# Kernel optimization log

Measured on AMD Instinct MI355X. Metric: run time of the kernel, lower is better.

## Reference

```python
import jax, jax.numpy as jnp
import numpy as np
import math

D_MODEL, N_HEADS, D_FF = 512, 8, 2048
B, S = 4, 2048
EPS = 1e-6


def _layernorm(x, alpha, bias):
    # Faithful to the torch module: std is unbiased (ddof=1) and eps is added to std, not var.
    m = jnp.mean(x, axis=-1, keepdims=True)
    s = jnp.std(x, axis=-1, keepdims=True, ddof=1)
    return alpha * (x - m) / (s + EPS) + bias


def setup_inputs() -> dict:
    key = jax.random.key(0)
    ks = jax.random.split(key, 16)
    d, f = D_MODEL, D_FF
    sd = 1.0 / math.sqrt(d)
    sf = 1.0 / math.sqrt(f)
    return {
        "x": jax.random.normal(ks[0], (B, S, d), jnp.float32),
        "wq": jax.random.normal(ks[1], (d, d), jnp.float32) * sd,
        "bq": jnp.zeros((d,), jnp.float32),
        "wk": jax.random.normal(ks[2], (d, d), jnp.float32) * sd,
        "bk": jnp.zeros((d,), jnp.float32),
        "wv": jax.random.normal(ks[3], (d, d), jnp.float32) * sd,
        "bv": jnp.zeros((d,), jnp.float32),
        "wo": jax.random.normal(ks[4], (d, d), jnp.float32) * sd,
        "bo": jnp.zeros((d,), jnp.float32),
        "w1": jax.random.normal(ks[5], (d, f), jnp.float32) * sd,
        "b1": jnp.zeros((f,), jnp.float32),
        "w2": jax.random.normal(ks[6], (f, d), jnp.float32) * sf,
        "b2": jnp.zeros((d,), jnp.float32),
        "ln1_a": jnp.ones((d,), jnp.float32),
        "ln1_b": jnp.zeros((d,), jnp.float32),
        "ln2_a": jnp.ones((d,), jnp.float32),
        "ln2_b": jnp.zeros((d,), jnp.float32),
    }


def reference(x, wq, bq, wk, bk, wv, bv, wo, bo, w1, b1, w2, b2, ln1_a, ln1_b, ln2_a, ln2_b):
    b, s, d = x.shape
    h, dk = N_HEADS, d // N_HEADS
    # QKV projections -> [b, h, s, dk]
    q = (x @ wq + bq).reshape(b, s, h, dk).transpose(0, 2, 1, 3)
    k = (x @ wk + bk).reshape(b, s, h, dk).transpose(0, 2, 1, 3)
    v = (x @ wv + bv).reshape(b, s, h, dk).transpose(0, 2, 1, 3)
    # Manual scaled-dot-product attention (no mask in EncoderBlock path)
    scores = jnp.einsum("bhqd,bhkd->bhqk", q, k) / jnp.sqrt(jnp.float32(dk))
    probs = jax.nn.softmax(scores, axis=-1)
    attn = jnp.einsum("bhqk,bhkd->bhqd", probs, v)
    concat = attn.transpose(0, 2, 1, 3).reshape(b, s, d)
    mha_out = concat @ wo + bo
    # Residual + LayerNorm 1
    y = _layernorm(x + mha_out, ln1_a, ln1_b)
    # FFN + Residual + LayerNorm 2
    ff = jax.nn.relu(y @ w1 + b1) @ w2 + b2
    return _layernorm(y + ff, ln2_a, ln2_b)
```

## Files before the change

kernel.cpp:

```cpp
#include <hip/hip_runtime.h>
#include <hip/hip_bf16.h>


typedef __bf16 bf16;
typedef __bf16 bf16x4 __attribute__((ext_vector_type(4)));
typedef __bf16 bf16x8 __attribute__((ext_vector_type(8)));
typedef float  f32x4  __attribute__((ext_vector_type(4)));

#define NBATCH 4
#define SEQ    2048
#define DMODEL 512
#define NHEADS 8
#define DHEAD  64
#define DFF    2048
#define MTOT   (NBATCH * SEQ)
#define WS_NEED 73416712u

__device__ __forceinline__ f32x4 mfma16(bf16x8 a, bf16x8 b, f32x4 c) {
    return __builtin_amdgcn_mfma_f32_16x16x32_bf16(a, b, c, 0, 0, 0);
}

__device__ __forceinline__ void lds16(const bf16* g, bf16* l) {
    __builtin_amdgcn_global_load_lds(
        (const __attribute__((address_space(1))) void*)g,
        (__attribute__((address_space(3))) void*)l, 16, 0, 0);
}

__device__ __forceinline__ float scrub(float f) {
    return (fabsf(f) < 1e30f) ? f : 0.f;
}

__global__ void sentinel_kernel(bf16* out) {
    out[threadIdx.x] = (bf16)1000.0f;
}

__global__ __launch_bounds__(256) void convert_x(
        const float* __restrict__ src, bf16* __restrict__ dst) {
    int i = (blockIdx.x * 256 + threadIdx.x) * 4;
    float4 f = *(const float4*)(src + i);
    bf16x4 o = {(bf16)scrub(f.x), (bf16)scrub(f.y),
                (bf16)scrub(f.z), (bf16)scrub(f.w)};
    *(bf16x4*)(dst + i) = o;
}

__global__ __launch_bounds__(256) void prep_kernel(
        const float* wq, const float* wk, const float* wv, const float* wo,
        const float* w1, const float* w2,
        const float* bq, const float* bk, const float* bv, const float* bo,
        const float* b1, const float* b2,
        const float* l1a, const float* l1b, const float* l2a, const float* l2b,
        bf16* __restrict__ wT, bf16* __restrict__ w1T, bf16* __restrict__ w2T,
        bf16* __restrict__ prm) {
    __shared__ bf16 tile[32][33];
    int b = blockIdx.x;
    if (b < 10) {
        const float* srcs[10] = {bq, bk, bv, bo, b1, b2, l1a, l1b, l2a, l2b};
        const int len[10] = {512,512,512,512,2048,512,512,512,512,512};
        const int dst[10] = {0,512,1024,1536,2048,4096,4608,5120,5632,6144};
        const float* s = srcs[b];
        bf16* d = prm + dst[b];
        for (int i = threadIdx.x; i < len[b]; i += 256)
            d[i] = (bf16)scrub(s[i]);
        return;
    }
    const float* in; bf16* out; int K, N, bx, by;
    if (b < 1034) {
        int idx = b - 10, z = idx >> 8, rem = idx & 255;
        const float* srcs[4] = {wq, wk, wv, wo};
        in = srcs[z]; out = wT + (size_t)z * 262144;
        K = 512; N = 512; bx = rem & 15; by = rem >> 4;
    } else if (b < 2058) {
        int idx = b - 1034;
        in = w1; out = w1T; K = 512; N = 2048; bx = idx & 63; by = idx >> 6;
    } else {
        int idx = b - 2058;
        in = w2; out = w2T; K = 2048; N = 512; bx = idx & 15; by = idx >> 4;
    }
    int tx = threadIdx.x & 31, ty = threadIdx.x >> 5;
    int n0 = bx * 32, k0 = by * 32;
#pragma unroll
    for (int i = 0; i < 4; i++) {
        int kl = ty * 4 + i;
        tile[kl][tx] = (bf16)scrub(in[(size_t)(k0 + kl) * N + n0 + tx]);
    }
    __syncthreads();
#pragma unroll
    for (int i = 0; i < 4; i++) {
        int nl = ty * 4 + i;
        out[(size_t)(n0 + nl) * K + k0 + tx] = tile[tx][nl];
    }
}

template <bool RELU>
__global__ __launch_bounds__(256) void gemm_bt(
        const bf16* __restrict__ A, const bf16* __restrict__ BT,
        const bf16* __restrict__ bias, bf16* __restrict__ Cout,
        int M, int N, int K) {
    constexpr int BM = 128, BN = 128, BK = 32;
    __shared__ __align__(16) bf16 As[BM * BK];
    __shared__ __align__(16) bf16 Bs[BN * BK];

    int tid  = threadIdx.x;
    int wid  = tid >> 6, lane = tid & 63;
    int quad = lane >> 4, l15 = lane & 15;
    int mb = blockIdx.x * BM, nb = blockIdx.y * BN;
    int wm = (wid >> 1) * 64, wn = (wid & 1) * 64;

    f32x4 acc[4][4] = {};

    int c0 = wid * 128 + lane, c1 = c0 + 64;
    int ar0 = c0 >> 2, ac0 = (c0 & 3) * 8;
    int ar1 = c1 >> 2, ac1 = (c1 & 3) * 8;
    bf16* lA0 = &As[(wid * 2 + 0) * 512];
    bf16* lA1 = &As[(wid * 2 + 1) * 512];
    bf16* lB0 = &Bs[(wid * 2 + 0) * 512];
    bf16* lB1 = &Bs[(wid * 2 + 1) * 512];

    for (int k0 = 0; k0 < K; k0 += BK) {
        __syncthreads();
        lds16(&A [(size_t)(mb + ar0) * K + k0 + ac0], lA0);
        lds16(&A [(size_t)(mb + ar1) * K + k0 + ac1], lA1);
        lds16(&BT[(size_t)(nb + ar0) * K + k0 + ac0], lB0);
        lds16(&BT[(size_t)(nb + ar1) * K + k0 + ac1], lB1);
        __syncthreads();

        bf16x8 af[4], bfr[4];
#pragma unroll
        for (int i = 0; i < 4; i++)
            af[i] = *(const bf16x8*)&As[(wm + i * 16 + l15) * 32 + quad * 8];
#pragma unroll
        for (int j = 0; j < 4; j++)
            bfr[j] = *(const bf16x8*)&Bs[(wn + j * 16 + l15) * 32 + quad * 8];
#pragma unroll
        for (int i = 0; i < 4; i++)
#pragma unroll
            for (int j = 0; j < 4; j++)
                acc[i][j] = mfma16(af[i], bfr[j], acc[i][j]);
    }

#pragma unroll
    for (int j = 0; j < 4; j++) {
        int n = nb + wn + j * 16 + l15;
        float bv = (float)bias[n];
#pragma unroll
        for (int i = 0; i < 4; i++) {
            int mBase = mb + wm + i * 16 + quad * 4;
#pragma unroll
            for (int r = 0; r < 4; r++) {
                float v = acc[i][j][r] + bv;
                if (RELU) v = v > 0.f ? v : 0.f;
                Cout[(size_t)(mBase + r) * N + n] = (bf16)v;
            }
        }
    }
}

template <bool RELU>
__global__ __launch_bounds__(256) void gemm_bt64(
        const bf16* __restrict__ A, const bf16* __restrict__ BT,
        const bf16* __restrict__ bias, bf16* __restrict__ Cout,
        int M, int N, int K) {
    constexpr int BM = 64, BN = 128, BK = 32;
    __shared__ __align__(16) bf16 As[BM * BK];
    __shared__ __align__(16) bf16 Bs[BN * BK];

    int tid  = threadIdx.x;
    int wid  = tid >> 6, lane = tid & 63;
    int quad = lane >> 4, l15 = lane & 15;
    int mb = blockIdx.x * BM, nb = blockIdx.y * BN;
    int wm = (wid >> 1) * 32, wn = (wid & 1) * 64;

    f32x4 acc[2][4] = {};

    int cA = wid * 64 + lane;
    int arA = cA >> 2, acA = (cA & 3) * 8;
    int cB0 = wid * 128 + lane, cB1 = cB0 + 64;
    int br0 = cB0 >> 2, bc0 = (cB0 & 3) * 8;
    int br1 = cB1 >> 2, bc1 = (cB1 & 3) * 8;
    bf16* lA  = &As[wid * 512];
    bf16* lB0 = &Bs[(wid * 2 + 0) * 512];
    bf16* lB1 = &Bs[(wid * 2 + 1) * 512];

    for (int k0 = 0; k0 < K; k0 += BK) {
        __syncthreads();
        lds16(&A [(size_t)(mb + arA) * K + k0 + acA], lA);
        lds16(&BT[(size_t)(nb + br0) * K + k0 + bc0], lB0);
        lds16(&BT[(size_t)(nb + br1) * K + k0 + bc1], lB1);
        __syncthreads();

        bf16x8 af[2], bfr[4];
#pragma unroll
        for (int i = 0; i < 2; i++)
            af[i] = *(const bf16x8*)&As[(wm + i * 16 + l15) * 32 + quad * 8];
#pragma unroll
        for (int j = 0; j < 4; j++)
            bfr[j] = *(const bf16x8*)&Bs[(wn + j * 16 + l15) * 32 + quad * 8];
#pragma unroll
        for (int i = 0; i < 2; i++)
#pragma unroll
            for (int j = 0; j < 4; j++)
                acc[i][j] = mfma16(af[i], bfr[j], acc[i][j]);
    }

#pragma unroll
    for (int j = 0; j < 4; j++) {
        int n = nb + wn + j * 16 + l15;
        float bv = (float)bias[n];
#pragma unroll
        for (int i = 0; i < 2; i++) {
            int mBase = mb + wm + i * 16 + quad * 4;
#pragma unroll
            for (int r = 0; r < 4; r++) {
                float v = acc[i][j][r] + bv;
                if (RELU) v = v > 0.f ? v : 0.f;
                Cout[(size_t)(mBase + r) * N + n] = (bf16)v;
            }
        }
    }
}

__global__ __launch_bounds__(256) void gemm_qkv(
        const bf16* __restrict__ A, const bf16* __restrict__ BT,
        const bf16* __restrict__ bias,
        bf16* __restrict__ Cq, bf16* __restrict__ Ck, bf16* __restrict__ Cv,
        int M, int N, int K) {
    constexpr int BM = 128, BN = 128, BK = 32;
    __shared__ __align__(16) bf16 As[BM * BK];
    __shared__ __align__(16) bf16 Bs[BN * BK];
    __shared__ __align__(16) bf16 Ts[128 * 136];

    int tid  = threadIdx.x;
    int wid  = tid >> 6, lane = tid & 63;
    int quad = lane >> 4, l15 = lane & 15;
    int mb = blockIdx.x * BM, nb = blockIdx.y * BN;
    int wm = (wid >> 1) * 64, wn = (wid & 1) * 64;

    f32x4 acc[4][4] = {};

    int c0 = wid * 128 + lane, c1 = c0 + 64;
    int ar0 = c0 >> 2, ac0 = (c0 & 3) * 8;
    int ar1 = c1 >> 2, ac1 = (c1 & 3) * 8;
    bf16* lA0 = &As[(wid * 2 + 0) * 512];
    bf16* lA1 = &As[(wid * 2 + 1) * 512];
    bf16* lB0 = &Bs[(wid * 2 + 0) * 512];
    bf16* lB1 = &Bs[(wid * 2 + 1) * 512];

    for (int k0 = 0; k0 < K; k0 += BK) {
        __syncthreads();
        lds16(&A [(size_t)(mb + ar0) * K + k0 + ac0], lA0);
        lds16(&A [(size_t)(mb + ar1) * K + k0 + ac1], lA1);
        lds16(&BT[(size_t)(nb + ar0) * K + k0 + ac0], lB0);
        lds16(&BT[(size_t)(nb + ar1) * K + k0 + ac1], lB1);
        __syncthreads();

        bf16x8 af[4], bfr[4];
#pragma unroll
        for (int i = 0; i < 4; i++)
            af[i] = *(const bf16x8*)&As[(wm + i * 16 + l15) * 32 + quad * 8];
#pragma unroll
        for (int j = 0; j < 4; j++)
            bfr[j] = *(const bf16x8*)&Bs[(wn + j * 16 + l15) * 32 + quad * 8];
#pragma unroll
        for (int i = 0; i < 4; i++)
#pragma unroll
            for (int j = 0; j < 4; j++)
                acc[i][j] = mfma16(af[i], bfr[j], acc[i][j]);
    }

    int reg = nb >> 9;
    if (reg < 2) {
        bf16* C = reg ? Ck : Cq;
        float scl = reg ? 1.0f : 0.125f;
#pragma unroll
        for (int j = 0; j < 4; j++) {
            int n = nb + wn + j * 16 + l15;
            float bv = (float)bias[n];
            int nn = n & 511;
            int h = nn >> 6, dk = nn & 63;
#pragma unroll
            for (int i = 0; i < 4; i++) {
                int mBase = mb + wm + i * 16 + quad * 4;
#pragma unroll
                for (int r = 0; r < 4; r++) {
                    float v = (acc[i][j][r] + bv) * scl;
                    int m = mBase + r;
                    int b = m >> 11, s = m & (SEQ - 1);
                    C[((size_t)(b * NHEADS + h) * SEQ + s) * DHEAD + dk] = (bf16)v;
                }
            }
        }
    } else {
#pragma unroll
        for (int j = 0; j < 4; j++) {
            int nl = wn + j * 16 + l15;
            float bv = (float)bias[nb + nl];
#pragma unroll
            for (int i = 0; i < 4; i++) {
                int ml = wm + i * 16 + quad * 4;
                bf16x4 pk;
#pragma unroll
                for (int r = 0; r < 4; r++) pk[r] = (bf16)(acc[i][j][r] + bv);
                *(bf16x4*)&Ts[nl * 136 + ml] = pk;
            }
        }
        __syncthreads();
        int nl = tid >> 1, half = tid & 1;
        int nn = (nb + nl) & 511;
        int h = nn >> 6, dk = nn & 63;
        int bb = mb >> 11, s0 = mb & (SEQ - 1);
        bf16* dst = &Cv[((size_t)(bb * NHEADS + h) * DHEAD + dk) * SEQ + s0 + half * 64];
        const bf16* srcl = &Ts[nl * 136 + half * 64];
#pragma unroll
        for (int v = 0; v < 8; v++)
            *(uint4*)(dst + v * 8) = *(const uint4*)(srcl + v * 8);
    }
}

__global__ __launch_bounds__(256) void attn_kernel(
        const bf16* __restrict__ Q, const bf16* __restrict__ K,
        const bf16* __restrict__ VT, bf16* __restrict__ Out) {
    __shared__ __align__(16) bf16 Ks[2][64 * 72];
    __shared__ __align__(16) bf16 Vs[2][64 * 72];
    __shared__ __align__(16) bf16 Pb[4][2][16 * 72];
    int tid  = threadIdx.x;
    int wid  = tid >> 6, lane = tid & 63;
    int quad = lane >> 4, l15 = lane & 15;
    int bh = blockIdx.y;
    int qb = blockIdx.x * 128 + wid * 32;

    const bf16* Qh = Q  + (size_t)bh * SEQ * DHEAD;
    const bf16* Kh = K  + (size_t)bh * SEQ * DHEAD;
    const bf16* Vh = VT + (size_t)bh * DHEAD * SEQ;

    bf16x8 bQ0[2], bQ1[2];
#pragma unroll
    for (int c = 0; c < 2; c++) {
        const bf16* qp = &Qh[(qb + c * 16 + l15) * DHEAD + quad * 8];
        bQ0[c] = *(const bf16x8*)qp;
        bQ1[c] = *(const bf16x8*)(qp + 32);
    }

    int cc0 = tid * 2, cc1 = cc0 + 1;
    int kr0 = cc0 >> 3, kc0 = (cc0 & 7) * 8;
    int kr1 = cc1 >> 3, kc1 = (cc1 & 7) * 8;

    float lrow[2] = {0.f, 0.f};
    f32x4 Oacc[2][4] = {};

    {
        uint4 ka0 = *(const uint4*)&Kh[(size_t)kr0 * DHEAD + kc0];
        uint4 ka1 = *(const uint4*)&Kh[(size_t)kr1 * DHEAD + kc1];
        uint4 va0 = *(const uint4*)&Vh[(size_t)kr0 * SEQ + kc0];
        uint4 va1 = *(const uint4*)&Vh[(size_t)kr1 * SEQ + kc1];
        *(uint4*)&Ks[0][kr0 * 72 + kc0] = ka0;
        *(uint4*)&Ks[0][kr1 * 72 + kc1] = ka1;
        *(uint4*)&Vs[0][kr0 * 72 + kc0] = va0;
        *(uint4*)&Vs[0][kr1 * 72 + kc1] = va1;
    }
    __syncthreads();

    for (int it = 0; it < SEQ / 64; it++) {
        int cur = it & 1, nxt = cur ^ 1;
        int kb = (it + 1) * 64;
        uint4 nk0, nk1, nv0, nv1;
        bool pf = (it + 1 < SEQ / 64);
        if (pf) {
            nk0 = *(const uint4*)&Kh[(size_t)(kb + kr0) * DHEAD + kc0];
            nk1 = *(const uint4*)&Kh[(size_t)(kb + kr1) * DHEAD + kc1];
            nv0 = *(const uint4*)&Vh[(size_t)kr0 * SEQ + kb + kc0];
            nv1 = *(const uint4*)&Vh[(size_t)kr1 * SEQ + kb + kc1];
        }

        bf16x8 aK0[4], aK1[4], bV0[4], bV1[4];
#pragma unroll
        for (int t = 0; t < 4; t++) {
            const bf16* kp = &Ks[cur][(t * 16 + l15) * 72 + quad * 8];
            aK0[t] = *(const bf16x8*)kp;
            aK1[t] = *(const bf16x8*)(kp + 32);
            const bf16* vp = &Vs[cur][(t * 16 + l15) * 72 + quad * 8];
            bV0[t] = *(const bf16x8*)vp;
            bV1[t] = *(const bf16x8*)(vp + 32);
        }

#pragma unroll
        for (int c = 0; c < 2; c++) {
            f32x4 st[4];
#pragma unroll
            for (int t = 0; t < 4; t++) {
                f32x4 z = {0.f, 0.f, 0.f, 0.f};
                st[t] = mfma16(aK1[t], bQ1[c], mfma16(aK0[t], bQ0[c], z));
            }
            bf16* myP = Pb[wid][c];
#pragma unroll
            for (int t = 0; t < 4; t++) {
                bf16x4 pk;
                float ps = 0.f;
#pragma unroll
                for (int r = 0; r < 4; r++) {
                    float p = __expf(fminf(st[t][r], 60.f));
                    ps += p;
                    pk[r] = (bf16)p;
                }
                lrow[c] += ps;
                *(bf16x4*)&myP[l15 * 72 + t * 16 + quad * 4] = pk;
            }
            bf16x8 aP0 = *(const bf16x8*)&myP[l15 * 72 + quad * 8];
            bf16x8 aP1 = *(const bf16x8*)&myP[l15 * 72 + 32 + quad * 8];
#pragma unroll
            for (int nt = 0; nt < 4; nt++)
                Oacc[c][nt] = mfma16(aP1, bV1[nt],
                                     mfma16(aP0, bV0[nt], Oacc[c][nt]));
        }

        if (pf) {
            *(uint4*)&Ks[nxt][kr0 * 72 + kc0] = nk0;
            *(uint4*)&Ks[nxt][kr1 * 72 + kc1] = nk1;
            *(uint4*)&Vs[nxt][kr0 * 72 + kc0] = nv0;
            *(uint4*)&Vs[nxt][kr1 * 72 + kc1] = nv1;
        }
        __syncthreads();
    }

    int b = bh >> 3, hd = bh & 7;
#pragma unroll
    for (int c = 0; c < 2; c++) {
        float l = lrow[c];
        l += __shfl_xor(l, 16);
        l += __shfl_xor(l, 32);
        float linv[4];
#pragma unroll
        for (int r = 0; r < 4; r++)
            linv[r] = 1.f / __shfl(l, quad * 4 + r);
#pragma unroll
        for (int nt = 0; nt < 4; nt++)
#pragma unroll
            for (int r = 0; r < 4; r++) {
                int s = qb + c * 16 + quad * 4 + r;
                Out[((size_t)(b * SEQ + s)) * DMODEL + hd * 64 + nt * 16 + l15]
                    = (bf16)(Oacc[c][nt][r] * linv[r]);
            }
    }
}

__global__ __launch_bounds__(256) void ln_kernel(
        const bf16* __restrict__ X, const bf16* __restrict__ T,
        const bf16* __restrict__ Al, const bf16* __restrict__ Bl,
        void* __restrict__ Out, int final_out) {
    int wid = threadIdx.x >> 6, lane = threadIdx.x & 63;
    int row = blockIdx.x * 4 + wid;
    const bf16* xr = X + (size_t)row * DMODEL;
    const bf16* tr = T + (size_t)row * DMODEL;
    bf16x8 xv = *(const bf16x8*)&xr[lane * 8];
    bf16x8 tv = *(const bf16x8*)&tr[lane * 8];
    float v[8];
#pragma unroll
    for (int i = 0; i < 8; i++) v[i] = (float)xv[i] + (float)tv[i];
    float sum = 0.f, sq = 0.f;
#pragma unroll
    for (int i = 0; i < 8; i++) { sum += v[i]; sq += v[i] * v[i]; }
#pragma unroll
    for (int m = 1; m < 64; m <<= 1) {
        sum += __shfl_xor(sum, m);
        sq  += __shfl_xor(sq,  m);
    }
    float mean = sum * (1.f / DMODEL);
    float var  = (sq - DMODEL * mean * mean) * (1.f / (DMODEL - 1));
    var = var > 0.f ? var : 0.f;
    float inv = 1.f / (sqrtf(var) + 1e-6f);
#pragma unroll
    for (int i = 0; i < 8; i++) {
        int c = lane * 8 + i;
        float yv = (float)Al[c] * (v[i] - mean) * inv + (float)Bl[c];
        yv = fminf(fmaxf(yv, -1e4f), 1e4f);
        size_t idx = (size_t)row * DMODEL + c;
        if (final_out) ((float*)Out)[idx] = yv;
        else           ((bf16*)Out)[idx]  = (bf16)yv;
    }
}

extern "C" void kernel_launch(void* const* d_in, const int* in_sizes, int n_in,
                              void* d_out, int out_size, void* d_ws, size_t ws_size,
                              hipStream_t stream) {
    if (ws_size < WS_NEED) {
        sentinel_kernel<<<1, 64, 0, stream>>>((bf16*)d_out);
        return;
    }

    const float* x  = (const float*)d_in[0];
    const float* wq = (const float*)d_in[1],  *bq = (const float*)d_in[2];
    const float* wk = (const float*)d_in[3],  *bk = (const float*)d_in[4];
    const float* wv = (const float*)d_in[5],  *bv = (const float*)d_in[6];
    const float* wo = (const float*)d_in[7],  *bo = (const float*)d_in[8];
    const float* w1 = (const float*)d_in[9],  *b1 = (const float*)d_in[10];
    const float* w2 = (const float*)d_in[11], *b2 = (const float*)d_in[12];
    const float* ln1a = (const float*)d_in[13], *ln1b = (const float*)d_in[14];
    const float* ln2a = (const float*)d_in[15], *ln2b = (const float*)d_in[16];

    char* ws = (char*)d_ws;
    bf16* wT   = (bf16*)(ws + 0);
    bf16* woT  = (bf16*)(ws + 1572864);
    bf16* w1T  = (bf16*)(ws + 2097152);
    bf16* w2T  = (bf16*)(ws + 4194304);
    bf16* xcv  = (bf16*)(ws + 6291456);
    bf16* prm  = (bf16*)(ws + 14680064);
    bf16* regA = (bf16*)(ws + 14696448);
    bf16* regB = (bf16*)(ws + 23085056);
    bf16* regC = (bf16*)(ws + 31473664);
    bf16* ff1  = (bf16*)(ws + 39862272);
    bf16* aout = (bf16*)d_out;

    bf16 *pbq = prm, *pbo = prm + 1536;
    bf16 *pb1 = prm + 2048, *pb2 = prm + 4096;
    bf16 *pl1a = prm + 4608, *pl1b = prm + 5120;
    bf16 *pl2a = prm + 5632, *pl2b = prm + 6144;

    convert_x<<<4096, 256, 0, stream>>>(x, xcv);
    prep_kernel<<<3082, 256, 0, stream>>>(wq, wk, wv, wo, w1, w2,
                                          bq, bk, bv, bo, b1, b2,
                                          ln1a, ln1b, ln2a, ln2b,
                                          wT, w1T, w2T, prm);

    gemm_qkv<<<dim3(64, 12), 256, 0, stream>>>(xcv, wT, pbq,
                                               regA, regB, regC,
                                               MTOT, 3 * DMODEL, DMODEL);

    attn_kernel<<<dim3(SEQ / 128, NBATCH * NHEADS), 256, 0, stream>>>(
        regA, regB, regC, aout);

    gemm_bt64<false><<<dim3(128, 4), 256, 0, stream>>>(aout, woT, pbo, regA,
                                                       MTOT, DMODEL, DMODEL);

    ln_kernel<<<MTOT / 4, 256, 0, stream>>>(xcv, regA, pl1a, pl1b, regB, 0);

    gemm_bt<true ><<<dim3(64, 16), 256, 0, stream>>>(regB, w1T, pb1, ff1,
                                                     MTOT, DFF, DMODEL);
    gemm_bt64<false><<<dim3(128, 4), 256, 0, stream>>>(ff1, w2T, pb2, regA,
                                                       MTOT, DMODEL, DFF);

    ln_kernel<<<MTOT / 4, 256, 0, stream>>>(regB, regA, pl2a, pl2b, d_out, 1);
}
```

Measured before the change: 293.0 us.

## Split attention across key halves with merge kernel, fuse x conversion, widen GEMM K-step

Attention now runs two blocks per query tile, each covering half the keys. They write unnormalised fp32 partial outputs and row sums, which a new merge kernel combines and normalises into bf16. The intent is to raise parallelism and occupancy in the attention stage, at the cost of extra fp32 partial traffic and one more launch. The x conversion is folded into the weight-prep kernel to save a launch. The bt64 GEMM loads 64-wide K slices per barrier pair to halve synchronisation.

```diff
diff --git a/kernel.cpp b/kernel.cpp
--- a/kernel.cpp
+++ b/kernel.cpp
@@ -14,7 +14,7 @@
 #define DHEAD  64
 #define DFF    2048
 #define MTOT   (NBATCH * SEQ)
-#define WS_NEED 73416712u
+#define WS_NEED 73940992u
 
 __device__ __forceinline__ f32x4 mfma16(bf16x8 a, bf16x8 b, f32x4 c) {
     return __builtin_amdgcn_mfma_f32_16x16x32_bf16(a, b, c, 0, 0, 0);
@@ -34,46 +34,48 @@
     out[threadIdx.x] = (bf16)1000.0f;
 }
 
-__global__ __launch_bounds__(256) void convert_x(
-        const float* __restrict__ src, bf16* __restrict__ dst) {
-    int i = (blockIdx.x * 256 + threadIdx.x) * 4;
-    float4 f = *(const float4*)(src + i);
-    bf16x4 o = {(bf16)scrub(f.x), (bf16)scrub(f.y),
-                (bf16)scrub(f.z), (bf16)scrub(f.w)};
-    *(bf16x4*)(dst + i) = o;
-}
-
 __global__ __launch_bounds__(256) void prep_kernel(
+        const float* x,
         const float* wq, const float* wk, const float* wv, const float* wo,
         const float* w1, const float* w2,
         const float* bq, const float* bk, const float* bv, const float* bo,
         const float* b1, const float* b2,
         const float* l1a, const float* l1b, const float* l2a, const float* l2b,
+        bf16* __restrict__ xcv,
         bf16* __restrict__ wT, bf16* __restrict__ w1T, bf16* __restrict__ w2T,
         bf16* __restrict__ prm) {
     __shared__ bf16 tile[32][33];
     int b = blockIdx.x;
-    if (b < 10) {
+    if (b < 4096) {
+        int i = (b * 256 + threadIdx.x) * 4;
+        float4 f = *(const float4*)(x + i);
+        bf16x4 o = {(bf16)scrub(f.x), (bf16)scrub(f.y),
+                    (bf16)scrub(f.z), (bf16)scrub(f.w)};
+        *(bf16x4*)(xcv + i) = o;
+        return;
+    }
+    if (b < 4106) {
+        int pb = b - 4096;
         const float* srcs[10] = {bq, bk, bv, bo, b1, b2, l1a, l1b, l2a, l2b};
         const int len[10] = {512,512,512,512,2048,512,512,512,512,512};
         const int dst[10] = {0,512,1024,1536,2048,4096,4608,5120,5632,6144};
-        const float* s = srcs[b];
-        bf16* d = prm + dst[b];
-        for (int i = threadIdx.x; i < len[b]; i += 256)
+        const float* s = srcs[pb];
+        bf16* d = prm + dst[pb];
+        for (int i = threadIdx.x; i < len[pb]; i += 256)
             d[i] = (bf16)scrub(s[i]);
         return;
     }
     const float* in; bf16* out; int K, N, bx, by;
-    if (b < 1034) {
-        int idx = b - 10, z = idx >> 8, rem = idx & 255;
+    if (b < 5130) {
+        int idx = b - 4106, z = idx >> 8, rem = idx & 255;
         const float* srcs[4] = {wq, wk, wv, wo};
         in = srcs[z]; out = wT + (size_t)z * 262144;
         K = 512; N = 512; bx = rem & 15; by = rem >> 4;
-    } else if (b < 2058) {
-        int idx = b - 1034;
+    } else if (b < 6154) {
+        int idx = b - 5130;
         in = w1; out = w1T; K = 512; N = 2048; bx = idx & 63; by = idx >> 6;
     } else {
-        int idx = b - 2058;
+        int idx = b - 6154;
         in = w2; out = w2T; K = 2048; N = 512; bx = idx & 15; by = idx >> 4;
     }
     int tx = threadIdx.x & 31, ty = threadIdx.x >> 5;
@@ -160,9 +162,9 @@
         const bf16* __restrict__ A, const bf16* __restrict__ BT,
         const bf16* __restrict__ bias, bf16* __restrict__ Cout,
         int M, int N, int K) {
-    constexpr int BM = 64, BN = 128, BK = 32;
-    __shared__ __align__(16) bf16 As[BM * BK];
-    __shared__ __align__(16) bf16 Bs[BN * BK];
+    constexpr int BM = 64, BN = 128;
+    __shared__ __align__(16) bf16 As0[BM * 32], As1[BM * 32];
+    __shared__ __align__(16) bf16 Bs0[BN * 32], Bs1[BN * 32];
 
     int tid  = threadIdx.x;
     int wid  = tid >> 6, lane = tid & 63;
@@ -177,29 +179,39 @@
     int cB0 = wid * 128 + lane, cB1 = cB0 + 64;
     int br0 = cB0 >> 2, bc0 = (cB0 & 3) * 8;
     int br1 = cB1 >> 2, bc1 = (cB1 & 3) * 8;
-    bf16* lA  = &As[wid * 512];
-    bf16* lB0 = &Bs[(wid * 2 + 0) * 512];
-    bf16* lB1 = &Bs[(wid * 2 + 1) * 512];
-
-    for (int k0 = 0; k0 < K; k0 += BK) {
-        __syncthreads();
-        lds16(&A [(size_t)(mb + arA) * K + k0 + acA], lA);
-        lds16(&BT[(size_t)(nb + br0) * K + k0 + bc0], lB0);
-        lds16(&BT[(size_t)(nb + br1) * K + k0 + bc1], lB1);
-        __syncthreads();
-
-        bf16x8 af[2], bfr[4];
+    bf16* lA0  = &As0[wid * 512];
+    bf16* lA1  = &As1[wid * 512];
+    bf16* lB00 = &Bs0[wid * 1024];
+    bf16* lB01 = &Bs0[wid * 1024 + 512];
+    bf16* lB10 = &Bs1[wid * 1024];
+    bf16* lB11 = &Bs1[wid * 1024 + 512];
+
+    for (int k0 = 0; k0 < K; k0 += 64) {
+        __syncthreads();
+        lds16(&A [(size_t)(mb + arA) * K + k0 + acA],      lA0);
+        lds16(&A [(size_t)(mb + arA) * K + k0 + 32 + acA], lA1);
+        lds16(&BT[(size_t)(nb + br0) * K + k0 + bc0],      lB00);
+        lds16(&BT[(size_t)(nb + br1) * K + k0 + bc1],      lB01);
+        lds16(&BT[(size_t)(nb + br0) * K + k0 + 32 + bc0], lB10);
+        lds16(&BT[(size_t)(nb + br1) * K + k0 + 32 + bc1], lB11);
+        __syncthreads();
+
+        bf16x8 a0[2], a1[2], b0[4], b1[4];
+#pragma unroll
+        for (int i = 0; i < 2; i++) {
+            a0[i] = *(const bf16x8*)&As0[(wm + i * 16 + l15) * 32 + quad * 8];
+            a1[i] = *(const bf16x8*)&As1[(wm + i * 16 + l15) * 32 + quad * 8];
+        }
+#pragma unroll
+        for (int j = 0; j < 4; j++) {
+            b0[j] = *(const bf16x8*)&Bs0[(wn + j * 16 + l15) * 32 + quad * 8];
+            b1[j] = *(const bf16x8*)&Bs1[(wn + j * 16 + l15) * 32 + quad * 8];
+        }
 #pragma unroll
         for (int i = 0; i < 2; i++)
-            af[i] = *(const bf16x8*)&As[(wm + i * 16 + l15) * 32 + quad * 8];
-#pragma unroll
-        for (int j = 0; j < 4; j++)
-            bfr[j] = *(const bf16x8*)&Bs[(wn + j * 16 + l15) * 32 + quad * 8];
-#pragma unroll
-        for (int i = 0; i < 2; i++)
 #pragma unroll
             for (int j = 0; j < 4; j++)
-                acc[i][j] = mfma16(af[i], bfr[j], acc[i][j]);
+                acc[i][j] = mfma16(a1[i], b1[j], mfma16(a0[i], b0[j], acc[i][j]));
     }
 
 #pragma unroll
@@ -318,15 +330,18 @@
 
 __global__ __launch_bounds__(256) void attn_kernel(
         const bf16* __restrict__ Q, const bf16* __restrict__ K,
-        const bf16* __restrict__ VT, bf16* __restrict__ Out) {
+        const bf16* __restrict__ VT,
+        float* __restrict__ Opart, float* __restrict__ lpart) {
     __shared__ __align__(16) bf16 Ks[2][64 * 72];
     __shared__ __align__(16) bf16 Vs[2][64 * 72];
-    __shared__ __align__(16) bf16 Pb[4][2][16 * 72];
+    __shared__ __align__(16) bf16 Pb[4][16 * 72];
     int tid  = threadIdx.x;
     int wid  = tid >> 6, lane = tid & 63;
     int quad = lane >> 4, l15 = lane & 15;
     int bh = blockIdx.y;
+    int z  = blockIdx.z;
     int qb = blockIdx.x * 128 + wid * 32;
+    int kb0 = z * (SEQ / 2);
 
     const bf16* Qh = Q  + (size_t)bh * SEQ * DHEAD;
     const bf16* Kh = K  + (size_t)bh * SEQ * DHEAD;
@@ -348,10 +363,10 @@
     f32x4 Oacc[2][4] = {};
 
     {
-        uint4 ka0 = *(const uint4*)&Kh[(size_t)kr0 * DHEAD + kc0];
-        uint4 ka1 = *(const uint4*)&Kh[(size_t)kr1 * DHEAD + kc1];
-        uint4 va0 = *(const uint4*)&Vh[(size_t)kr0 * SEQ + kc0];
-        uint4 va1 = *(const uint4*)&Vh[(size_t)kr1 * SEQ + kc1];
+        uint4 ka0 = *(const uint4*)&Kh[(size_t)(kb0 + kr0) * DHEAD + kc0];
+        uint4 ka1 = *(const uint4*)&Kh[(size_t)(kb0 + kr1) * DHEAD + kc1];
+        uint4 va0 = *(const uint4*)&Vh[(size_t)kr0 * SEQ + kb0 + kc0];
+        uint4 va1 = *(const uint4*)&Vh[(size_t)kr1 * SEQ + kb0 + kc1];
         *(uint4*)&Ks[0][kr0 * 72 + kc0] = ka0;
         *(uint4*)&Ks[0][kr1 * 72 + kc1] = ka1;
         *(uint4*)&Vs[0][kr0 * 72 + kc0] = va0;
@@ -359,11 +374,11 @@
     }
     __syncthreads();
 
-    for (int it = 0; it < SEQ / 64; it++) {
+    for (int it = 0; it < 16; it++) {
         int cur = it & 1, nxt = cur ^ 1;
-        int kb = (it + 1) * 64;
+        int kb = kb0 + (it + 1) * 64;
         uint4 nk0, nk1, nv0, nv1;
-        bool pf = (it + 1 < SEQ / 64);
+        bool pf = (it + 1 < 16);
         if (pf) {
             nk0 = *(const uint4*)&Kh[(size_t)(kb + kr0) * DHEAD + kc0];
             nk1 = *(const uint4*)&Kh[(size_t)(kb + kr1) * DHEAD + kc1];
@@ -387,10 +402,10 @@
             f32x4 st[4];
 #pragma unroll
             for (int t = 0; t < 4; t++) {
-                f32x4 z = {0.f, 0.f, 0.f, 0.f};
-                st[t] = mfma16(aK1[t], bQ1[c], mfma16(aK0[t], bQ0[c], z));
-            }
-            bf16* myP = Pb[wid][c];
+                f32x4 zv = {0.f, 0.f, 0.f, 0.f};
+                st[t] = mfma16(aK1[t], bQ1[c], mfma16(aK0[t], bQ0[c], zv));
+            }
+            bf16* myP = Pb[wid];
 #pragma unroll
             for (int t = 0; t < 4; t++) {
                 bf16x4 pk;
@@ -422,24 +437,40 @@
     }
 
     int b = bh >> 3, hd = bh & 7;
+    float* Op = Opart + (size_t)z * (MTOT * (size_t)DMODEL);
 #pragma unroll
     for (int c = 0; c < 2; c++) {
         float l = lrow[c];
         l += __shfl_xor(l, 16);
         l += __shfl_xor(l, 32);
-        float linv[4];
-#pragma unroll
-        for (int r = 0; r < 4; r++)
-            linv[r] = 1.f / __shfl(l, quad * 4 + r);
+        if (quad == 0)
+            lpart[z * 65536 + bh * SEQ + qb + c * 16 + l15] = l;
 #pragma unroll
         for (int nt = 0; nt < 4; nt++)
 #pragma unroll
             for (int r = 0; r < 4; r++) {
                 int s = qb + c * 16 + quad * 4 + r;
-                Out[((size_t)(b * SEQ + s)) * DMODEL + hd * 64 + nt * 16 + l15]
-                    = (bf16)(Oacc[c][nt][r] * linv[r]);
-            }
-    }
+                Op[((size_t)(b * SEQ + s)) * DMODEL + hd * 64 + nt * 16 + l15]
+                    = Oacc[c][nt][r];
+            }
+    }
+}
+
+__global__ __launch_bounds__(256) void merge_o(
+        const float* __restrict__ Opart, const float* __restrict__ lpart,
+        bf16* __restrict__ Out) {
+    int idx4 = blockIdx.x * 256 + threadIdx.x;
+    int e = idx4 * 4;
+    int sg = e >> 9, col = e & 511;
+    int b = sg >> 11, s = sg & (SEQ - 1), hd = col >> 6;
+    int li = (b * NHEADS + hd) * SEQ + s;
+    float linv = 1.f / (lpart[li] + lpart[65536 + li]);
+    f32x4 o0 = ((const f32x4*)Opart)[idx4];
+    f32x4 o1 = ((const f32x4*)(Opart + (size_t)MTOT * DMODEL))[idx4];
+    bf16x4 o;
+#pragma unroll
+    for (int r = 0; r < 4; r++) o[r] = (bf16)((o0[r] + o1[r]) * linv);
+    *(bf16x4*)(Out + e) = o;
 }
 
 __global__ __launch_bounds__(256) void ln_kernel(
@@ -507,6 +538,8 @@
     bf16* regB = (bf16*)(ws + 23085056);
     bf16* regC = (bf16*)(ws + 31473664);
     bf16* ff1  = (bf16*)(ws + 39862272);
+    float* Opart = (float*)(ws + 39862272);
+    float* lpart = (float*)(ws + 73416704);
     bf16* aout = (bf16*)d_out;
 
     bf16 *pbq = prm, *pbo = prm + 1536;
@@ -514,18 +547,18 @@
     bf16 *pl1a = prm + 4608, *pl1b = prm + 5120;
     bf16 *pl2a = prm + 5632, *pl2b = prm + 6144;
 
-    convert_x<<<4096, 256, 0, stream>>>(x, xcv);
-    prep_kernel<<<3082, 256, 0, stream>>>(wq, wk, wv, wo, w1, w2,
+    prep_kernel<<<7178, 256, 0, stream>>>(x, wq, wk, wv, wo, w1, w2,
                                           bq, bk, bv, bo, b1, b2,
                                           ln1a, ln1b, ln2a, ln2b,
-                                          wT, w1T, w2T, prm);
+                                          xcv, wT, w1T, w2T, prm);
 
     gemm_qkv<<<dim3(64, 12), 256, 0, stream>>>(xcv, wT, pbq,
                                                regA, regB, regC,
                                                MTOT, 3 * DMODEL, DMODEL);
 
-    attn_kernel<<<dim3(SEQ / 128, NBATCH * NHEADS), 256, 0, stream>>>(
-        regA, regB, regC, aout);
+    attn_kernel<<<dim3(SEQ / 128, NBATCH * NHEADS, 2), 256, 0, stream>>>(
+        regA, regB, regC, Opart, lpart);
+    merge_o<<<4096, 256, 0, stream>>>(Opart, lpart, aout);
 
     gemm_bt64<false><<<dim3(128, 4), 256, 0, stream>>>(aout, woT, pbo, regA,
                                                        MTOT, DMODEL, DMODEL);
```

After: 294.1 us. About the same (+0.4%).
